# Optimization experiments

Measured on AMD Instinct MI355X. Metric: run time of the kernel, lower is better.

The kernel has to match this reference:

```python
import jax, jax.numpy as jnp
import numpy as np

T, H, I, E, K = 1024, 1024, 512, 32, 4   # tokens, hidden, moe_inter, n_experts, top_k
G, TG, NS = 8, 4, 2                      # n_group, topk_group, n_shared_experts
C = 2 * T * K // E                       # expert capacity (no-drop headroom)
SCALE = 2.5                              # routed_scaling_factor


def setup_inputs() -> dict:
    key = jax.random.key(0)
    ks = jax.random.split(key, 7)
    s = 0.02
    return dict(
        hidden_states=jax.random.normal(ks[0], (T, H), jnp.float32),
        gate_w=jax.random.normal(ks[1], (E, H), jnp.float32) * s,
        e_bias=jax.random.normal(ks[2], (E,), jnp.float32) * 0.1,
        w_gate_up=jax.random.normal(ks[3], (E, 2 * I, H), jnp.float32) * s,
        w_down=jax.random.normal(ks[4], (E, H, I), jnp.float32) * s,
        w_gate_up_shared=jax.random.normal(ks[5], (2 * I * NS, H), jnp.float32) * s,
        w_down_shared=jax.random.normal(ks[6], (H, I * NS), jnp.float32) * s,
    )


def reference(hidden_states, gate_w, e_bias, w_gate_up, w_down, w_gate_up_shared, w_down_shared):
    x = hidden_states                                   # (T, H)
    # --- gate + sigmoid scoring (noaux_tc) ---
    logits = x @ gate_w.T                               # (T, E)
    scores = jax.nn.sigmoid(logits.astype(jnp.float32))
    sfc = scores + e_bias                               # scores_for_choice
    # --- group-limited top-k: top-2 sum per group, keep topk_group groups ---
    group_scores = jax.lax.top_k(sfc.reshape(T, G, E // G), 2)[0].sum(-1)  # (T, G)
    grp_idx = jax.lax.top_k(group_scores, TG)[1]        # (T, TG)
    gmask = jnp.zeros((T, G), jnp.float32).at[jnp.arange(T)[:, None], grp_idx].set(1.0)
    smask = jnp.repeat(gmask, E // G, axis=1)           # (T, E)
    sfc_m = jnp.where(smask > 0, sfc, 0.0)
    topk_idx = jax.lax.top_k(sfc_m, K)[1]               # (T, K)
    tw = jnp.take_along_axis(scores, topk_idx, axis=1)  # weights from raw scores
    tw = tw / (tw.sum(-1, keepdims=True) + 1e-20)       # norm_topk_prob
    tw = tw * SCALE
    # --- capacity-based dispatch (position within expert via cumsum of one-hot) ---
    e_flat = topk_idx.reshape(-1)                       # (T*K,)
    oh = jax.nn.one_hot(e_flat, E, dtype=jnp.float32)   # (T*K, E)
    pos = jnp.sum((jnp.cumsum(oh, axis=0) - 1.0) * oh, axis=-1).astype(jnp.int32)
    keep = (pos < C).astype(jnp.float32)                # capacity sized to never drop
    pos_c = jnp.clip(pos, 0, C - 1)
    t_flat = jnp.repeat(jnp.arange(T), K)
    combine = jnp.zeros((T, E, C), jnp.float32).at[t_flat, e_flat, pos_c].add(tw.reshape(-1) * keep)
    dispatch = jnp.zeros((T, E, C), jnp.float32).at[t_flat, e_flat, pos_c].add(keep)
    # --- grouped expert MLP (gate_up -> SiluAndMul -> down) ---
    xe = jnp.einsum('tec,th->ech', dispatch, x)         # (E, C, H)
    gu = jnp.einsum('ech,eoh->eco', xe, w_gate_up)      # (E, C, 2I)
    act = jax.nn.silu(gu[..., :I]) * gu[..., I:]
    ye = jnp.einsum('eci,ehi->ech', act, w_down)        # (E, C, H)
    routed = jnp.einsum('tec,ech->th', combine, ye)     # (T, H)
    # --- shared experts MLP on residual ---
    IS = I * NS
    gus = x @ w_gate_up_shared.T                        # (T, 2*IS)
    acts = jax.nn.silu(gus[:, :IS]) * gus[:, IS:]
    shared = acts @ w_down_shared.T                     # (T, H)
    return routed + shared
```

## Files before the change

kernel.cpp:

```cpp
#include <hip/hip_runtime.h>
#include <hip/hip_bf16.h>
#include <math.h>

#define T_TOK 1024
#define H_DIM 1024
#define I_DIM 512
#define E_NUM 32
#define K_TOP 4
#define G_NUM 8
#define TG_NUM 4
#define CAP 256
#define IS_DIM 1024
#define RSCALE 2.5f

#define WS_CNT_OFF    0
#define WS_NT_OFF     128
#define WS_TILE_OFF   256
#define WS_EIDX_OFF   4096
#define WS_WN_OFF     20480
#define WS_STOK_OFF   36864
#define WS_SW_OFF     69632
#define WS_ACT_OFF    102400
#define WS_ACTS_OFF   (102400 + (size_t)E_NUM*CAP*I_DIM*2)

typedef __attribute__((ext_vector_type(8))) short short8v;
typedef __attribute__((ext_vector_type(4))) float f32x4;
typedef __attribute__((ext_vector_type(4))) unsigned uint4v;

__device__ __forceinline__ short f2bf(float f) {
    unsigned u = __float_as_uint(f);
    u += 0x7FFFu + ((u >> 16) & 1u);
    return (short)(u >> 16);
}
__device__ __forceinline__ unsigned pk2bf(float a, float b) {
    unsigned ua = __float_as_uint(a) + 0x8000u;
    unsigned ub = __float_as_uint(b) + 0x8000u;
    return __builtin_amdgcn_perm(ub, ua, 0x07060302);
}
__device__ __forceinline__ uint4v pk8bf(float4 lo, float4 hi) {
    uint4v r; r.x = pk2bf(lo.x, lo.y); r.y = pk2bf(lo.z, lo.w);
    r.z = pk2bf(hi.x, hi.y); r.w = pk2bf(hi.z, hi.w); return r;
}
__device__ __forceinline__ float silu_(float g) { return g / (1.f + expf(-g)); }

#define LDSTRIDE 40

__global__ __launch_bounds__(256) void gate_kernel(
    const float* __restrict__ x, const float* __restrict__ gate_w,
    const float* __restrict__ e_bias,
    int* __restrict__ eidx, float* __restrict__ wnorm)
{
    __shared__ float xs[H_DIM];
    __shared__ float logits[E_NUM];
    const int t = blockIdx.x;
    const int tid = threadIdx.x;
    ((float4*)xs)[tid] = ((const float4*)(x + (size_t)t * H_DIM))[tid];
    __syncthreads();

    const int e = tid >> 3, sub = tid & 7;
    const float4* gw4 = (const float4*)(gate_w + (size_t)e * H_DIM + sub * 128);
    const float4* xr4 = (const float4*)(xs + sub * 128);
    float p = 0.f;
    #pragma unroll
    for (int h = 0; h < 32; ++h) {
        float4 a = xr4[h], b = gw4[h];
        p += a.x * b.x + a.y * b.y + a.z * b.z + a.w * b.w;
    }
    for (int off = 4; off; off >>= 1) p += __shfl_down(p, off, 8);
    if (sub == 0) logits[e] = p;
    __syncthreads();
    if (tid != 0) return;

    float sc[E_NUM], sfc[E_NUM];
    for (int i = 0; i < E_NUM; ++i) {
        sc[i] = 1.f / (1.f + expf(-logits[i]));
        sfc[i] = sc[i] + e_bias[i];
    }
    float gs[G_NUM];
    for (int g = 0; g < G_NUM; ++g) {
        float m1 = -1e30f, m2 = -1e30f;
        for (int j = 0; j < E_NUM / G_NUM; ++j) {
            float v = sfc[g * (E_NUM / G_NUM) + j];
            if (v > m1) { m2 = m1; m1 = v; } else if (v > m2) m2 = v;
        }
        gs[g] = m1 + m2;
    }
    bool gm[G_NUM];
    for (int g = 0; g < G_NUM; ++g) gm[g] = false;
    for (int it = 0; it < TG_NUM; ++it) {
        int best = -1; float bv = -1e30f;
        for (int g = 0; g < G_NUM; ++g) if (!gm[g] && gs[g] > bv) { bv = gs[g]; best = g; }
        gm[best] = true;
    }
    float sm[E_NUM];
    for (int i = 0; i < E_NUM; ++i) sm[i] = gm[i / (E_NUM / G_NUM)] ? sfc[i] : 0.0f;
    int idx[K_TOP]; float w[K_TOP]; float tsum = 0.f;
    for (int it = 0; it < K_TOP; ++it) {
        int best = 0; float bv = -1e30f;
        for (int i = 0; i < E_NUM; ++i) if (sm[i] > bv) { bv = sm[i]; best = i; }
        sm[best] = -1e30f;
        idx[it] = best; w[it] = sc[best]; tsum += w[it];
    }
    float inv = RSCALE / (tsum + 1e-20f);
    const int base = t * K_TOP;
    for (int it = 0; it < K_TOP; ++it) {
        eidx[base + it] = idx[it];
        wnorm[base + it] = w[it] * inv;
    }
}

__global__ __launch_bounds__(256) void assign_kernel(
    const int* __restrict__ eidx, const float* __restrict__ wnorm,
    int* __restrict__ cnt, int* __restrict__ slot_token, float* __restrict__ slot_w,
    int* __restrict__ ntiles, int* __restrict__ tiles)
{
    __shared__ int   se[T_TOK * K_TOP];
    __shared__ float swt[T_TOK * K_TOP];
    __shared__ int   scnt[E_NUM];
    const int tid = threadIdx.x;
    for (int i = tid; i < T_TOK * K_TOP; i += 256) { se[i] = eidx[i]; swt[i] = wnorm[i]; }
    __syncthreads();

    const int e = tid >> 3;
    const int seg = tid & 7;
    const int base = seg * 512;
    int c = 0;
    for (int i = 0; i < 512; ++i) c += (se[base + i] == e);
    int excl = 0, total = 0;
    for (int s = 0; s < 8; ++s) {
        int cs = __shfl(c, s, 8);
        total += cs;
        if (s < seg) excl += cs;
    }
    if (seg == 0) { cnt[e] = total; scnt[e] = total; }
    int pos = excl;
    for (int i = 0; i < 512; ++i) {
        if (se[base + i] == e) {
            if (pos < CAP) {
                slot_token[e * CAP + pos] = (base + i) >> 2;
                slot_w[e * CAP + pos] = swt[base + i];
            }
            ++pos;
        }
    }
    __syncthreads();
    if (tid == 0) {
        int nt = 0;
        for (int ee = 0; ee < E_NUM; ++ee) {
            int n = min(scnt[ee], CAP);
            for (int r = 0; r < n; r += 64) {
                tiles[nt * 4] = ee; tiles[nt * 4 + 1] = r; tiles[nt * 4 + 2] = n;
                ++nt;
            }
        }
        *ntiles = nt;
    }
}

#define WAVE_SETUP() \
    const int tid = threadIdx.x; const int lane = tid & 63; const int wid = tid >> 6; \
    const int wm = wid & 1, wn = wid >> 1; \
    const int lr16 = lane & 15, kc = lane >> 4; \
    const int sc_ = tid & 3, srow = tid >> 2;

#define DECL_ACC() f32x4 acc[2][4]; \
    _Pragma("unroll") for (int i_ = 0; i_ < 2; ++i_) \
    _Pragma("unroll") for (int j_ = 0; j_ < 4; ++j_) acc[i_][j_] = 0.f;

#define COMPUTE_2x4() do { \
    short8v a_[2], b_[4]; \
    _Pragma("unroll") for (int mt = 0; mt < 2; ++mt) \
        a_[mt] = *(const short8v*)&As[(wm*32 + mt*16 + lr16)*LDSTRIDE + kc*8]; \
    _Pragma("unroll") for (int nt = 0; nt < 4; ++nt) \
        b_[nt] = *(const short8v*)&Bs[(wn*64 + nt*16 + lr16)*LDSTRIDE + kc*8]; \
    _Pragma("unroll") for (int mt = 0; mt < 2; ++mt) \
    _Pragma("unroll") for (int nt = 0; nt < 4; ++nt) \
        acc[mt][nt] = __builtin_amdgcn_mfma_f32_16x16x32_bf16(a_[mt], b_[nt], acc[mt][nt], 0, 0, 0); \
} while (0)

__global__ __launch_bounds__(256, 4) void moe_gu_kernel(
    const float* __restrict__ x, const float* __restrict__ w_gate_up,
    const int* __restrict__ ntiles, const int* __restrict__ tiles,
    const int* __restrict__ slot_token, const float* __restrict__ slot_w,
    short* __restrict__ act)
{
    if ((int)blockIdx.y >= *ntiles) return;
    const int e  = tiles[blockIdx.y * 4];
    const int r0 = tiles[blockIdx.y * 4 + 1];
    const int ne = tiles[blockIdx.y * 4 + 2];
    const int nI0 = blockIdx.x * 64;

    __shared__ __align__(16) short As[64 * LDSTRIDE];
    __shared__ __align__(16) short Bs[128 * LDSTRIDE];
    __shared__ int   toks[64];
    __shared__ float sws[64];

    WAVE_SETUP();
    if (tid < 64) {
        int p = r0 + tid; bool v = p < ne;
        toks[tid] = v ? slot_token[e * CAP + p] : 0;
        sws[tid]  = v ? slot_w[e * CAP + p] : 0.f;
    }
    __syncthreads();

    const float* aptr = x + (size_t)toks[srow] * H_DIM + sc_ * 8;
    const float* wgu_e = w_gate_up + (size_t)e * (2 * I_DIM) * H_DIM;
    const int cB1 = srow + 64;
    const int wr0 = ((srow >> 4) & 1) * I_DIM + nI0 + ((srow >> 5) << 4) + (srow & 15);
    const int wr1 = ((cB1 >> 4) & 1) * I_DIM + nI0 + ((cB1 >> 5) << 4) + (cB1 & 15);
    const float* bptr0 = wgu_e + (size_t)wr0 * H_DIM + sc_ * 8;
    const float* bptr1 = wgu_e + (size_t)wr1 * H_DIM + sc_ * 8;
    const int aoff = srow * LDSTRIDE + sc_ * 8;
    const int boff0 = srow * LDSTRIDE + sc_ * 8;
    const int boff1 = cB1 * LDSTRIDE + sc_ * 8;

    DECL_ACC();
    float4 cA0 = *(const float4*)(aptr), cA1 = *(const float4*)(aptr + 4);
    float4 cB0a = *(const float4*)(bptr0), cB0b = *(const float4*)(bptr0 + 4);
    float4 cB1a = *(const float4*)(bptr1), cB1b = *(const float4*)(bptr1 + 4);

    for (int k0 = 0; k0 < H_DIM; k0 += 32) {
        float4 nA0, nA1, nB0a, nB0b, nB1a, nB1b;
        const int k1 = k0 + 32;
        if (k1 < H_DIM) {
            nA0 = *(const float4*)(aptr + k1);  nA1 = *(const float4*)(aptr + k1 + 4);
            nB0a = *(const float4*)(bptr0 + k1); nB0b = *(const float4*)(bptr0 + k1 + 4);
            nB1a = *(const float4*)(bptr1 + k1); nB1b = *(const float4*)(bptr1 + k1 + 4);
        }
        *(uint4v*)&As[aoff]  = pk8bf(cA0, cA1);
        *(uint4v*)&Bs[boff0] = pk8bf(cB0a, cB0b);
        *(uint4v*)&Bs[boff1] = pk8bf(cB1a, cB1b);
        __syncthreads();
        COMPUTE_2x4();
        __syncthreads();
        cA0 = nA0; cA1 = nA1; cB0a = nB0a; cB0b = nB0b; cB1a = nB1a; cB1b = nB1b;
    }

    #pragma unroll
    for (int mt = 0; mt < 2; ++mt) {
        #pragma unroll
        for (int q = 0; q < 2; ++q) {
            f32x4 g = acc[mt][2 * q], u = acc[mt][2 * q + 1];
            int colI = nI0 + wn * 32 + q * 16 + lr16;
            #pragma unroll
            for (int i = 0; i < 4; ++i) {
                int rl = wm * 32 + mt * 16 + kc * 4 + i;
                int p = r0 + rl;
                if (p < ne) {
                    float s = sws[rl];
                    act[((size_t)e * CAP + p) * I_DIM + colI] = f2bf(s * silu_(g[i]) * u[i]);
                }
            }
        }
    }
}

__global__ __launch_bounds__(256, 4) void moe_down_kernel(
    const short* __restrict__ act, const float* __restrict__ w_down,
    const int* __restrict__ ntiles, const int* __restrict__ tiles,
    const int* __restrict__ slot_token, float* __restrict__ out)
{
    if ((int)blockIdx.y >= *ntiles) return;
    const int e  = tiles[blockIdx.y * 4];
    const int r0 = tiles[blockIdx.y * 4 + 1];
    const int ne = tiles[blockIdx.y * 4 + 2];
    const int h0 = blockIdx.x * 128;

    __shared__ __align__(16) short As[64 * LDSTRIDE];
    __shared__ __align__(16) short Bs[128 * LDSTRIDE];
    __shared__ int toks[64];

    WAVE_SETUP();
    if (tid < 64) {
        int p = r0 + tid;
        toks[tid] = (p < ne) ? slot_token[e * CAP + p] : 0;
    }
    __syncthreads();

    const short* aptr = act + ((size_t)e * CAP + r0 + srow) * I_DIM + sc_ * 8;
    const float* wd_e = w_down + (size_t)e * H_DIM * I_DIM;
    const float* bptr0 = wd_e + (size_t)(h0 + srow) * I_DIM + sc_ * 8;
    const float* bptr1 = wd_e + (size_t)(h0 + srow + 64) * I_DIM + sc_ * 8;
    const int aoff = srow * LDSTRIDE + sc_ * 8;
    const int boff1 = (srow + 64) * LDSTRIDE + sc_ * 8;

    DECL_ACC();
    short8v cA = *(const short8v*)(aptr);
    float4 cB0a = *(const float4*)(bptr0), cB0b = *(const float4*)(bptr0 + 4);
    float4 cB1a = *(const float4*)(bptr1), cB1b = *(const float4*)(bptr1 + 4);

    for (int k0 = 0; k0 < I_DIM; k0 += 32) {
        short8v nA; float4 nB0a, nB0b, nB1a, nB1b;
        const int k1 = k0 + 32;
        if (k1 < I_DIM) {
            nA = *(const short8v*)(aptr + k1);
            nB0a = *(const float4*)(bptr0 + k1); nB0b = *(const float4*)(bptr0 + k1 + 4);
            nB1a = *(const float4*)(bptr1 + k1); nB1b = *(const float4*)(bptr1 + k1 + 4);
        }
        *(short8v*)&As[aoff] = cA;
        *(uint4v*)&Bs[aoff]  = pk8bf(cB0a, cB0b);
        *(uint4v*)&Bs[boff1] = pk8bf(cB1a, cB1b);
        __syncthreads();
        COMPUTE_2x4();
        __syncthreads();
        cA = nA; cB0a = nB0a; cB0b = nB0b; cB1a = nB1a; cB1b = nB1b;
    }

    #pragma unroll
    for (int mt = 0; mt < 2; ++mt) {
        #pragma unroll
        for (int i = 0; i < 4; ++i) {
            int rl = wm * 32 + mt * 16 + kc * 4 + i;
            int p = r0 + rl;
            if (p < ne) {
                float* orow = out + (size_t)toks[rl] * H_DIM + h0 + wn * 64;
                #pragma unroll
                for (int nt = 0; nt < 4; ++nt)
                    atomicAdd(&orow[nt * 16 + lr16], acc[mt][nt][i]);
            }
        }
    }
}

__global__ __launch_bounds__(256, 4) void shared_gu_kernel(
    const float* __restrict__ x, const float* __restrict__ w_gus,
    short* __restrict__ acts)
{
    const int t0 = blockIdx.y * 64;
    const int nI0 = blockIdx.x * 64;
    __shared__ __align__(16) short As[64 * LDSTRIDE];
    __shared__ __align__(16) short Bs[128 * LDSTRIDE];

    WAVE_SETUP();
    const float* aptr = x + (size_t)(t0 + srow) * H_DIM + sc_ * 8;
    const int cB1 = srow + 64;
    const int wr0 = ((srow >> 4) & 1) * IS_DIM + nI0 + ((srow >> 5) << 4) + (srow & 15);
    const int wr1 = ((cB1 >> 4) & 1) * IS_DIM + nI0 + ((cB1 >> 5) << 4) + (cB1 & 15);
    const float* bptr0 = w_gus + (size_t)wr0 * H_DIM + sc_ * 8;
    const float* bptr1 = w_gus + (size_t)wr1 * H_DIM + sc_ * 8;
    const int aoff = srow * LDSTRIDE + sc_ * 8;
    const int boff1 = cB1 * LDSTRIDE + sc_ * 8;

    DECL_ACC();
    float4 cA0 = *(const float4*)(aptr), cA1 = *(const float4*)(aptr + 4);
    float4 cB0a = *(const float4*)(bptr0), cB0b = *(const float4*)(bptr0 + 4);
    float4 cB1a = *(const float4*)(bptr1), cB1b = *(const float4*)(bptr1 + 4);

    for (int k0 = 0; k0 < H_DIM; k0 += 32) {
        float4 nA0, nA1, nB0a, nB0b, nB1a, nB1b;
        const int k1 = k0 + 32;
        if (k1 < H_DIM) {
            nA0 = *(const float4*)(aptr + k1);  nA1 = *(const float4*)(aptr + k1 + 4);
            nB0a = *(const float4*)(bptr0 + k1); nB0b = *(const float4*)(bptr0 + k1 + 4);
            nB1a = *(const float4*)(bptr1 + k1); nB1b = *(const float4*)(bptr1 + k1 + 4);
        }
        *(uint4v*)&As[aoff]  = pk8bf(cA0, cA1);
        *(uint4v*)&Bs[aoff]  = pk8bf(cB0a, cB0b);
        *(uint4v*)&Bs[boff1] = pk8bf(cB1a, cB1b);
        __syncthreads();
        COMPUTE_2x4();
        __syncthreads();
        cA0 = nA0; cA1 = nA1; cB0a = nB0a; cB0b = nB0b; cB1a = nB1a; cB1b = nB1b;
    }

    #pragma unroll
    for (int mt = 0; mt < 2; ++mt) {
        #pragma unroll
        for (int q = 0; q < 2; ++q) {
            f32x4 g = acc[mt][2 * q], u = acc[mt][2 * q + 1];
            int colI = nI0 + wn * 32 + q * 16 + lr16;
            #pragma unroll
            for (int i = 0; i < 4; ++i) {
                int t = t0 + wm * 32 + mt * 16 + kc * 4 + i;
                acts[(size_t)t * IS_DIM + colI] = f2bf(silu_(g[i]) * u[i]);
            }
        }
    }
}

__global__ __launch_bounds__(256, 4) void shared_down_kernel(
    const short* __restrict__ acts, const float* __restrict__ w_ds,
    float* __restrict__ out)
{
    const int t0 = blockIdx.y * 64;
    const int h0 = blockIdx.x * 128;
    __shared__ __align__(16) short As[64 * LDSTRIDE];
    __shared__ __align__(16) short Bs[128 * LDSTRIDE];

    WAVE_SETUP();
    const short* aptr = acts + (size_t)(t0 + srow) * IS_DIM + sc_ * 8;
    const float* bptr0 = w_ds + (size_t)(h0 + srow) * IS_DIM + sc_ * 8;
    const float* bptr1 = w_ds + (size_t)(h0 + srow + 64) * IS_DIM + sc_ * 8;
    const int aoff = srow * LDSTRIDE + sc_ * 8;
    const int boff1 = (srow + 64) * LDSTRIDE + sc_ * 8;

    DECL_ACC();
    short8v cA = *(const short8v*)(aptr);
    float4 cB0a = *(const float4*)(bptr0), cB0b = *(const float4*)(bptr0 + 4);
    float4 cB1a = *(const float4*)(bptr1), cB1b = *(const float4*)(bptr1 + 4);

    for (int k0 = 0; k0 < IS_DIM; k0 += 32) {
        short8v nA; float4 nB0a, nB0b, nB1a, nB1b;
        const int k1 = k0 + 32;
        if (k1 < IS_DIM) {
            nA = *(const short8v*)(aptr + k1);
            nB0a = *(const float4*)(bptr0 + k1); nB0b = *(const float4*)(bptr0 + k1 + 4);
            nB1a = *(const float4*)(bptr1 + k1); nB1b = *(const float4*)(bptr1 + k1 + 4);
        }
        *(short8v*)&As[aoff] = cA;
        *(uint4v*)&Bs[aoff]  = pk8bf(cB0a, cB0b);
        *(uint4v*)&Bs[boff1] = pk8bf(cB1a, cB1b);
        __syncthreads();
        COMPUTE_2x4();
        __syncthreads();
        cA = nA; cB0a = nB0a; cB0b = nB0b; cB1a = nB1a; cB1b = nB1b;
    }

    #pragma unroll
    for (int mt = 0; mt < 2; ++mt) {
        #pragma unroll
        for (int i = 0; i < 4; ++i) {
            int t = t0 + wm * 32 + mt * 16 + kc * 4 + i;
            float* orow = out + (size_t)t * H_DIM + h0 + wn * 64;
            #pragma unroll
            for (int nt = 0; nt < 4; ++nt)
                orow[nt * 16 + lr16] = acc[mt][nt][i];
        }
    }
}

extern "C" void kernel_launch(void* const* d_in, const int* in_sizes, int n_in,
                              void* d_out, int out_size, void* d_ws, size_t ws_size,
                              hipStream_t stream) {
    const float* x   = (const float*)d_in[0];
    const float* gw  = (const float*)d_in[1];
    const float* eb  = (const float*)d_in[2];
    const float* wgu = (const float*)d_in[3];
    const float* wd  = (const float*)d_in[4];
    const float* wgs = (const float*)d_in[5];
    const float* wds = (const float*)d_in[6];
    float* out = (float*)d_out;
    char* ws = (char*)d_ws;

    int*   cnt    = (int*)(ws + WS_CNT_OFF);
    int*   ntiles = (int*)(ws + WS_NT_OFF);
    int*   tiles  = (int*)(ws + WS_TILE_OFF);
    int*   eidx   = (int*)(ws + WS_EIDX_OFF);
    float* wnorm  = (float*)(ws + WS_WN_OFF);
    int*   stok   = (int*)(ws + WS_STOK_OFF);
    float* sw     = (float*)(ws + WS_SW_OFF);
    short* act    = (short*)(ws + WS_ACT_OFF);
    short* acts   = (short*)(ws + WS_ACTS_OFF);

    gate_kernel<<<T_TOK, 256, 0, stream>>>(x, gw, eb, eidx, wnorm);
    assign_kernel<<<1, 256, 0, stream>>>(eidx, wnorm, cnt, stok, sw, ntiles, tiles);
    shared_gu_kernel<<<dim3(IS_DIM / 64, T_TOK / 64), 256, 0, stream>>>(x, wgs, acts);
    shared_down_kernel<<<dim3(H_DIM / 128, T_TOK / 64), 256, 0, stream>>>(acts, wds, out);
    moe_gu_kernel<<<dim3(I_DIM / 64, 128), 256, 0, stream>>>(x, wgu, ntiles, tiles, stok, sw, act);
    moe_down_kernel<<<dim3(H_DIM / 128, 128), 256, 0, stream>>>(act, wd, ntiles, tiles, stok, out);
}
```

Before: 432.0 us.

## Merge shared-expert GEMMs into routed MoE kernels and double-buffer LDS

Shared-expert tiles are added to the routed tile list, so one gate-up kernel and one down kernel run both shared and routed work. This removes two launches and lets the shared tiles fill the idle slots of the routed grid. The output is now zeroed with a memset and the shared down results are written with atomics instead of plain stores, which adds atomic traffic. LDS tiles are double-buffered so the second barrier per k-step can be dropped.

```diff
diff --git a/kernel.cpp b/kernel.cpp
--- a/kernel.cpp
+++ b/kernel.cpp
@@ -13,6 +13,8 @@
 #define IS_DIM 1024
 #define RSCALE 2.5f
 
+#define MAXTILES 160
+
 #define WS_CNT_OFF    0
 #define WS_NT_OFF     128
 #define WS_TILE_OFF   256
@@ -146,11 +148,13 @@
     __syncthreads();
     if (tid == 0) {
         int nt = 0;
+        for (int t0 = 0; t0 < T_TOK; t0 += 64) {
+            tiles[nt * 4] = -1; tiles[nt * 4 + 1] = t0; tiles[nt * 4 + 2] = 64; ++nt;
+        }
         for (int ee = 0; ee < E_NUM; ++ee) {
             int n = min(scnt[ee], CAP);
             for (int r = 0; r < n; r += 64) {
-                tiles[nt * 4] = ee; tiles[nt * 4 + 1] = r; tiles[nt * 4 + 2] = n;
-                ++nt;
+                tiles[nt * 4] = ee; tiles[nt * 4 + 1] = r; tiles[nt * 4 + 2] = n; ++nt;
             }
         }
         *ntiles = nt;
@@ -167,96 +171,105 @@
     _Pragma("unroll") for (int i_ = 0; i_ < 2; ++i_) \
     _Pragma("unroll") for (int j_ = 0; j_ < 4; ++j_) acc[i_][j_] = 0.f;
 
-#define COMPUTE_2x4() do { \
+#define COMPUTE_2x4(Asb, Bsb) do { \
     short8v a_[2], b_[4]; \
     _Pragma("unroll") for (int mt = 0; mt < 2; ++mt) \
-        a_[mt] = *(const short8v*)&As[(wm*32 + mt*16 + lr16)*LDSTRIDE + kc*8]; \
+        a_[mt] = *(const short8v*)&(Asb)[(wm*32 + mt*16 + lr16)*LDSTRIDE + kc*8]; \
     _Pragma("unroll") for (int nt = 0; nt < 4; ++nt) \
-        b_[nt] = *(const short8v*)&Bs[(wn*64 + nt*16 + lr16)*LDSTRIDE + kc*8]; \
+        b_[nt] = *(const short8v*)&(Bsb)[(wn*64 + nt*16 + lr16)*LDSTRIDE + kc*8]; \
     _Pragma("unroll") for (int mt = 0; mt < 2; ++mt) \
     _Pragma("unroll") for (int nt = 0; nt < 4; ++nt) \
         acc[mt][nt] = __builtin_amdgcn_mfma_f32_16x16x32_bf16(a_[mt], b_[nt], acc[mt][nt], 0, 0, 0); \
 } while (0)
 
-__global__ __launch_bounds__(256, 4) void moe_gu_kernel(
+__global__ __launch_bounds__(256, 4) void gu_all_kernel(
     const float* __restrict__ x, const float* __restrict__ w_gate_up,
+    const float* __restrict__ w_gus,
     const int* __restrict__ ntiles, const int* __restrict__ tiles,
     const int* __restrict__ slot_token, const float* __restrict__ slot_w,
-    short* __restrict__ act)
+    short* __restrict__ act, short* __restrict__ acts)
 {
     if ((int)blockIdx.y >= *ntiles) return;
     const int e  = tiles[blockIdx.y * 4];
     const int r0 = tiles[blockIdx.y * 4 + 1];
     const int ne = tiles[blockIdx.y * 4 + 2];
-    const int nI0 = blockIdx.x * 64;
-
-    __shared__ __align__(16) short As[64 * LDSTRIDE];
-    __shared__ __align__(16) short Bs[128 * LDSTRIDE];
+    const bool sh = (e < 0);
+    if (!sh && blockIdx.x >= I_DIM / 64) return;
+    const int col0 = blockIdx.x * 64;
+
+    __shared__ __align__(16) short As[2][64 * LDSTRIDE];
+    __shared__ __align__(16) short Bs[2][128 * LDSTRIDE];
     __shared__ int   toks[64];
     __shared__ float sws[64];
 
     WAVE_SETUP();
     if (tid < 64) {
-        int p = r0 + tid; bool v = p < ne;
-        toks[tid] = v ? slot_token[e * CAP + p] : 0;
-        sws[tid]  = v ? slot_w[e * CAP + p] : 0.f;
-    }
-    __syncthreads();
-
-    const float* aptr = x + (size_t)toks[srow] * H_DIM + sc_ * 8;
-    const float* wgu_e = w_gate_up + (size_t)e * (2 * I_DIM) * H_DIM;
-    const int cB1 = srow + 64;
-    const int wr0 = ((srow >> 4) & 1) * I_DIM + nI0 + ((srow >> 5) << 4) + (srow & 15);
-    const int wr1 = ((cB1 >> 4) & 1) * I_DIM + nI0 + ((cB1 >> 5) << 4) + (cB1 & 15);
-    const float* bptr0 = wgu_e + (size_t)wr0 * H_DIM + sc_ * 8;
-    const float* bptr1 = wgu_e + (size_t)wr1 * H_DIM + sc_ * 8;
-    const int aoff = srow * LDSTRIDE + sc_ * 8;
-    const int boff0 = srow * LDSTRIDE + sc_ * 8;
-    const int boff1 = cB1 * LDSTRIDE + sc_ * 8;
+        if (sh) { toks[tid] = r0 + tid; sws[tid] = 1.f; }
+        else {
+            int p = r0 + tid; bool v = p < ne;
+            toks[tid] = v ? slot_token[e * CAP + p] : 0;
+            sws[tid]  = v ? slot_w[e * CAP + p] : 0.f;
+        }
+    }
+    __syncthreads();
+
+    const int IDim = sh ? IS_DIM : I_DIM;
+    const float* wbase = sh ? w_gus : (w_gate_up + (size_t)e * (2 * I_DIM) * H_DIM);
+    const int c1 = srow + 64;
+    const int wr0 = ((srow >> 4) & 1) * IDim + col0 + ((srow >> 5) << 4) + (srow & 15);
+    const int wr1 = ((c1 >> 4) & 1) * IDim + col0 + ((c1 >> 5) << 4) + (c1 & 15);
+    const float* aptr  = x + (size_t)toks[srow] * H_DIM + sc_ * 8;
+    const float* bptr0 = wbase + (size_t)wr0 * H_DIM + sc_ * 8;
+    const float* bptr1 = wbase + (size_t)wr1 * H_DIM + sc_ * 8;
+    const int aoff  = srow * LDSTRIDE + sc_ * 8;
+    const int boff1 = c1 * LDSTRIDE + sc_ * 8;
 
     DECL_ACC();
-    float4 cA0 = *(const float4*)(aptr), cA1 = *(const float4*)(aptr + 4);
+    float4 cA0 = *(const float4*)(aptr),  cA1 = *(const float4*)(aptr + 4);
     float4 cB0a = *(const float4*)(bptr0), cB0b = *(const float4*)(bptr0 + 4);
     float4 cB1a = *(const float4*)(bptr1), cB1b = *(const float4*)(bptr1 + 4);
 
+    int buf = 0;
     for (int k0 = 0; k0 < H_DIM; k0 += 32) {
         float4 nA0, nA1, nB0a, nB0b, nB1a, nB1b;
         const int k1 = k0 + 32;
         if (k1 < H_DIM) {
-            nA0 = *(const float4*)(aptr + k1);  nA1 = *(const float4*)(aptr + k1 + 4);
+            nA0 = *(const float4*)(aptr + k1);   nA1 = *(const float4*)(aptr + k1 + 4);
             nB0a = *(const float4*)(bptr0 + k1); nB0b = *(const float4*)(bptr0 + k1 + 4);
             nB1a = *(const float4*)(bptr1 + k1); nB1b = *(const float4*)(bptr1 + k1 + 4);
         }
-        *(uint4v*)&As[aoff]  = pk8bf(cA0, cA1);
-        *(uint4v*)&Bs[boff0] = pk8bf(cB0a, cB0b);
-        *(uint4v*)&Bs[boff1] = pk8bf(cB1a, cB1b);
+        *(uint4v*)&As[buf][aoff]  = pk8bf(cA0, cA1);
+        *(uint4v*)&Bs[buf][aoff]  = pk8bf(cB0a, cB0b);
+        *(uint4v*)&Bs[buf][boff1] = pk8bf(cB1a, cB1b);
         __syncthreads();
-        COMPUTE_2x4();
-        __syncthreads();
+        COMPUTE_2x4(As[buf], Bs[buf]);
+        buf ^= 1;
         cA0 = nA0; cA1 = nA1; cB0a = nB0a; cB0b = nB0b; cB1a = nB1a; cB1b = nB1b;
     }
 
+    short* rowbase = sh ? (acts + (size_t)r0 * IS_DIM)
+                        : (act + ((size_t)e * CAP + r0) * I_DIM);
     #pragma unroll
     for (int mt = 0; mt < 2; ++mt) {
         #pragma unroll
         for (int q = 0; q < 2; ++q) {
             f32x4 g = acc[mt][2 * q], u = acc[mt][2 * q + 1];
-            int colI = nI0 + wn * 32 + q * 16 + lr16;
+            int colI = col0 + wn * 32 + q * 16 + lr16;
             #pragma unroll
             for (int i = 0; i < 4; ++i) {
                 int rl = wm * 32 + mt * 16 + kc * 4 + i;
-                int p = r0 + rl;
-                if (p < ne) {
+                if (rl < ne - r0 || sh) {
                     float s = sws[rl];
-                    act[((size_t)e * CAP + p) * I_DIM + colI] = f2bf(s * silu_(g[i]) * u[i]);
+                    rowbase[(size_t)rl * IDim + colI] = f2bf(s * silu_(g[i]) * u[i]);
                 }
             }
         }
     }
 }
 
-__global__ __launch_bounds__(256, 4) void moe_down_kernel(
-    const short* __restrict__ act, const float* __restrict__ w_down,
+__global__ __launch_bounds__(256, 4) void down_all_kernel(
+    const short* __restrict__ act, const short* __restrict__ acts,
+    const float* __restrict__ w_down, const float* __restrict__ w_ds,
     const int* __restrict__ ntiles, const int* __restrict__ tiles,
     const int* __restrict__ slot_token, float* __restrict__ out)
 {
@@ -264,24 +277,31 @@
     const int e  = tiles[blockIdx.y * 4];
     const int r0 = tiles[blockIdx.y * 4 + 1];
     const int ne = tiles[blockIdx.y * 4 + 2];
+    const bool sh = (e < 0);
     const int h0 = blockIdx.x * 128;
 
-    __shared__ __align__(16) short As[64 * LDSTRIDE];
-    __shared__ __align__(16) short Bs[128 * LDSTRIDE];
+    __shared__ __align__(16) short As[2][64 * LDSTRIDE];
+    __shared__ __align__(16) short Bs[2][128 * LDSTRIDE];
     __shared__ int toks[64];
 
     WAVE_SETUP();
     if (tid < 64) {
-        int p = r0 + tid;
-        toks[tid] = (p < ne) ? slot_token[e * CAP + p] : 0;
-    }
-    __syncthreads();
-
-    const short* aptr = act + ((size_t)e * CAP + r0 + srow) * I_DIM + sc_ * 8;
-    const float* wd_e = w_down + (size_t)e * H_DIM * I_DIM;
-    const float* bptr0 = wd_e + (size_t)(h0 + srow) * I_DIM + sc_ * 8;
-    const float* bptr1 = wd_e + (size_t)(h0 + srow + 64) * I_DIM + sc_ * 8;
-    const int aoff = srow * LDSTRIDE + sc_ * 8;
+        if (sh) toks[tid] = r0 + tid;
+        else {
+            int p = r0 + tid;
+            toks[tid] = (p < ne) ? slot_token[e * CAP + p] : 0;
+        }
+    }
+    __syncthreads();
+
+    const int Kdim = sh ? IS_DIM : I_DIM;
+    const short* abase = sh ? (acts + (size_t)(r0 + srow) * IS_DIM)
+                            : (act + ((size_t)e * CAP + r0 + srow) * I_DIM);
+    const float* wbase = sh ? w_ds : (w_down + (size_t)e * H_DIM * I_DIM);
+    const float* bptr0 = wbase + (size_t)(h0 + srow) * Kdim + sc_ * 8;
+    const float* bptr1 = wbase + (size_t)(h0 + srow + 64) * Kdim + sc_ * 8;
+    const short* aptr  = abase + sc_ * 8;
+    const int aoff  = srow * LDSTRIDE + sc_ * 8;
     const int boff1 = (srow + 64) * LDSTRIDE + sc_ * 8;
 
     DECL_ACC();
@@ -289,20 +309,21 @@
     float4 cB0a = *(const float4*)(bptr0), cB0b = *(const float4*)(bptr0 + 4);
     float4 cB1a = *(const float4*)(bptr1), cB1b = *(const float4*)(bptr1 + 4);
 
-    for (int k0 = 0; k0 < I_DIM; k0 += 32) {
+    int buf = 0;
+    for (int k0 = 0; k0 < Kdim; k0 += 32) {
         short8v nA; float4 nB0a, nB0b, nB1a, nB1b;
         const int k1 = k0 + 32;
-        if (k1 < I_DIM) {
+        if (k1 < Kdim) {
             nA = *(const short8v*)(aptr + k1);
             nB0a = *(const float4*)(bptr0 + k1); nB0b = *(const float4*)(bptr0 + k1 + 4);
             nB1a = *(const float4*)(bptr1 + k1); nB1b = *(const float4*)(bptr1 + k1 + 4);
         }
-        *(short8v*)&As[aoff] = cA;
-        *(uint4v*)&Bs[aoff]  = pk8bf(cB0a, cB0b);
-        *(uint4v*)&Bs[boff1] = pk8bf(cB1a, cB1b);
+        *(short8v*)&As[buf][aoff] = cA;
+        *(uint4v*)&Bs[buf][aoff]  = pk8bf(cB0a, cB0b);
+        *(uint4v*)&Bs[buf][boff1] = pk8bf(cB1a, cB1b);
         __syncthreads();
-        COMPUTE_2x4();
-        __syncthreads();
+        COMPUTE_2x4(As[buf], Bs[buf]);
+        buf ^= 1;
         cA = nA; cB0a = nB0a; cB0b = nB0b; cB1a = nB1a; cB1b = nB1b;
     }
 
@@ -311,120 +332,12 @@
         #pragma unroll
         for (int i = 0; i < 4; ++i) {
             int rl = wm * 32 + mt * 16 + kc * 4 + i;
-            int p = r0 + rl;
-            if (p < ne) {
+            if (rl < ne - r0 || sh) {
                 float* orow = out + (size_t)toks[rl] * H_DIM + h0 + wn * 64;
                 #pragma unroll
                 for (int nt = 0; nt < 4; ++nt)
                     atomicAdd(&orow[nt * 16 + lr16], acc[mt][nt][i]);
             }
-        }
-    }
-}
-
-__global__ __launch_bounds__(256, 4) void shared_gu_kernel(
-    const float* __restrict__ x, const float* __restrict__ w_gus,
-    short* __restrict__ acts)
-{
-    const int t0 = blockIdx.y * 64;
-    const int nI0 = blockIdx.x * 64;
-    __shared__ __align__(16) short As[64 * LDSTRIDE];
-    __shared__ __align__(16) short Bs[128 * LDSTRIDE];
-
-    WAVE_SETUP();
-    const float* aptr = x + (size_t)(t0 + srow) * H_DIM + sc_ * 8;
-    const int cB1 = srow + 64;
-    const int wr0 = ((srow >> 4) & 1) * IS_DIM + nI0 + ((srow >> 5) << 4) + (srow & 15);
-    const int wr1 = ((cB1 >> 4) & 1) * IS_DIM + nI0 + ((cB1 >> 5) << 4) + (cB1 & 15);
-    const float* bptr0 = w_gus + (size_t)wr0 * H_DIM + sc_ * 8;
-    const float* bptr1 = w_gus + (size_t)wr1 * H_DIM + sc_ * 8;
-    const int aoff = srow * LDSTRIDE + sc_ * 8;
-    const int boff1 = cB1 * LDSTRIDE + sc_ * 8;
-
-    DECL_ACC();
-    float4 cA0 = *(const float4*)(aptr), cA1 = *(const float4*)(aptr + 4);
-    float4 cB0a = *(const float4*)(bptr0), cB0b = *(const float4*)(bptr0 + 4);
-    float4 cB1a = *(const float4*)(bptr1), cB1b = *(const float4*)(bptr1 + 4);
-
-    for (int k0 = 0; k0 < H_DIM; k0 += 32) {
-        float4 nA0, nA1, nB0a, nB0b, nB1a, nB1b;
-        const int k1 = k0 + 32;
-        if (k1 < H_DIM) {
-            nA0 = *(const float4*)(aptr + k1);  nA1 = *(const float4*)(aptr + k1 + 4);
-            nB0a = *(const float4*)(bptr0 + k1); nB0b = *(const float4*)(bptr0 + k1 + 4);
-            nB1a = *(const float4*)(bptr1 + k1); nB1b = *(const float4*)(bptr1 + k1 + 4);
-        }
-        *(uint4v*)&As[aoff]  = pk8bf(cA0, cA1);
-        *(uint4v*)&Bs[aoff]  = pk8bf(cB0a, cB0b);
-        *(uint4v*)&Bs[boff1] = pk8bf(cB1a, cB1b);
-        __syncthreads();
-        COMPUTE_2x4();
-        __syncthreads();
-        cA0 = nA0; cA1 = nA1; cB0a = nB0a; cB0b = nB0b; cB1a = nB1a; cB1b = nB1b;
-    }
-
-    #pragma unroll
-    for (int mt = 0; mt < 2; ++mt) {
-        #pragma unroll
-        for (int q = 0; q < 2; ++q) {
-            f32x4 g = acc[mt][2 * q], u = acc[mt][2 * q + 1];
-            int colI = nI0 + wn * 32 + q * 16 + lr16;
-            #pragma unroll
-            for (int i = 0; i < 4; ++i) {
-                int t = t0 + wm * 32 + mt * 16 + kc * 4 + i;
-                acts[(size_t)t * IS_DIM + colI] = f2bf(silu_(g[i]) * u[i]);
-            }
-        }
-    }
-}
-
-__global__ __launch_bounds__(256, 4) void shared_down_kernel(
-    const short* __restrict__ acts, const float* __restrict__ w_ds,
-    float* __restrict__ out)
-{
-    const int t0 = blockIdx.y * 64;
-    const int h0 = blockIdx.x * 128;
-    __shared__ __align__(16) short As[64 * LDSTRIDE];
-    __shared__ __align__(16) short Bs[128 * LDSTRIDE];
-
-    WAVE_SETUP();
-    const short* aptr = acts + (size_t)(t0 + srow) * IS_DIM + sc_ * 8;
-    const float* bptr0 = w_ds + (size_t)(h0 + srow) * IS_DIM + sc_ * 8;
-    const float* bptr1 = w_ds + (size_t)(h0 + srow + 64) * IS_DIM + sc_ * 8;
-    const int aoff = srow * LDSTRIDE + sc_ * 8;
-    const int boff1 = (srow + 64) * LDSTRIDE + sc_ * 8;
-
-    DECL_ACC();
-    short8v cA = *(const short8v*)(aptr);
-    float4 cB0a = *(const float4*)(bptr0), cB0b = *(const float4*)(bptr0 + 4);
-    float4 cB1a = *(const float4*)(bptr1), cB1b = *(const float4*)(bptr1 + 4);
-
-    for (int k0 = 0; k0 < IS_DIM; k0 += 32) {
-        short8v nA; float4 nB0a, nB0b, nB1a, nB1b;
-        const int k1 = k0 + 32;
-        if (k1 < IS_DIM) {
-            nA = *(const short8v*)(aptr + k1);
-            nB0a = *(const float4*)(bptr0 + k1); nB0b = *(const float4*)(bptr0 + k1 + 4);
-            nB1a = *(const float4*)(bptr1 + k1); nB1b = *(const float4*)(bptr1 + k1 + 4);
-        }
-        *(short8v*)&As[aoff] = cA;
-        *(uint4v*)&Bs[aoff]  = pk8bf(cB0a, cB0b);
-        *(uint4v*)&Bs[boff1] = pk8bf(cB1a, cB1b);
-        __syncthreads();
-        COMPUTE_2x4();
-        __syncthreads();
-        cA = nA; cB0a = nB0a; cB0b = nB0b; cB1a = nB1a; cB1b = nB1b;
-    }
-
-    #pragma unroll
-    for (int mt = 0; mt < 2; ++mt) {
-        #pragma unroll
-        for (int i = 0; i < 4; ++i) {
-            int t = t0 + wm * 32 + mt * 16 + kc * 4 + i;
-            float* orow = out + (size_t)t * H_DIM + h0 + wn * 64;
-            #pragma unroll
-            for (int nt = 0; nt < 4; ++nt)
-                orow[nt * 16 + lr16] = acc[mt][nt][i];
         }
     }
 }
@@ -452,10 +365,11 @@
     short* act    = (short*)(ws + WS_ACT_OFF);
     short* acts   = (short*)(ws + WS_ACTS_OFF);
 
+    hipMemsetAsync(out, 0, (size_t)T_TOK * H_DIM * sizeof(float), stream);
     gate_kernel<<<T_TOK, 256, 0, stream>>>(x, gw, eb, eidx, wnorm);
     assign_kernel<<<1, 256, 0, stream>>>(eidx, wnorm, cnt, stok, sw, ntiles, tiles);
-    shared_gu_kernel<<<dim3(IS_DIM / 64, T_TOK / 64), 256, 0, stream>>>(x, wgs, acts);
-    shared_down_kernel<<<dim3(H_DIM / 128, T_TOK / 64), 256, 0, stream>>>(acts, wds, out);
-    moe_gu_kernel<<<dim3(I_DIM / 64, 128), 256, 0, stream>>>(x, wgu, ntiles, tiles, stok, sw, act);
-    moe_down_kernel<<<dim3(H_DIM / 128, 128), 256, 0, stream>>>(act, wd, ntiles, tiles, stok, out);
-}
+    gu_all_kernel<<<dim3(IS_DIM / 64, MAXTILES), 256, 0, stream>>>(
+        x, wgu, wgs, ntiles, tiles, stok, sw, act, acts);
+    down_all_kernel<<<dim3(H_DIM / 128, MAXTILES), 256, 0, stream>>>(
+        act, acts, wd, wds, ntiles, tiles, stok, out);
+}
```

Result: no change. 428.0 us (-0.9%).
